# Performance work log

Measured on AMD Instinct MI355X. Metric: run time of the kernel, lower is better.

## Reference

```python
import jax, jax.numpy as jnp
import numpy as np

# Paged/ragged causal prefill attention (FlashInfer wrapper.run semantics),
# modeled as equal-length batched causal GQA attention.
B, S = 2, 2048          # batch, seq_len (T = B*S tokens, flattened)
H, HKV, D = 32, 8, 128  # query heads, kv heads, head dim
G = H // HKV            # GQA group size
SCALE = 0.08838834764831845  # 1/sqrt(D)


def setup_inputs() -> dict:
    key = jax.random.key(0)
    kq, kk, kv = jax.random.split(key, 3)
    q = jax.random.normal(kq, (B * S, H * D), dtype=jnp.float32)
    k = jax.random.normal(kk, (B * S, HKV * D), dtype=jnp.float32)
    v = jax.random.normal(kv, (B * S, HKV * D), dtype=jnp.float32)
    return {"q": q, "k": k, "v": v}


def reference(q, k, v):
    # q: [T, H*D] -> [B, S, HKV, G, D]; k, v: [T, HKV*D] -> [B, S, HKV, D]
    qh = q.reshape(B, S, HKV, G, D)
    kh = k.reshape(B, S, HKV, D)
    vh = v.reshape(B, S, HKV, D)
    # GQA attention scores: [B, HKV, G, Sq, Sk]
    scores = jnp.einsum('bqhgd,bkhd->bhgqk', qh, kh) * SCALE
    causal = jnp.tril(jnp.ones((S, S), dtype=bool))  # query attends to keys <= its position
    scores = jnp.where(causal, scores, jnp.finfo(scores.dtype).min)
    probs = jax.nn.softmax(scores, axis=-1)
    out = jnp.einsum('bhgqk,bkhd->bqhgd', probs, vh)
    # back to flattened token layout [T, H*D]
    return out.reshape(B * S, H * D)
```

## Files before the change

### kernel.cpp

```cpp
#include <hip/hip_runtime.h>


#define B_   2
#define S_   2048
#define H_   32
#define HKV_ 8
#define D_   128
#define SCALEF 0.08838834764831845f
#define COEF  (SCALEF * 1.44269504088896340736f)
#define DEFER_THR 8.0f

typedef float          f32x4 __attribute__((ext_vector_type(4)));
typedef __bf16         bf16x2 __attribute__((ext_vector_type(2)));
typedef __bf16         bf16x8 __attribute__((ext_vector_type(8)));
typedef unsigned short u16x8 __attribute__((ext_vector_type(8)));

#define MFMA16(a, b, c) __builtin_amdgcn_mfma_f32_16x16x32_bf16((a), (b), (c), 0, 0, 0)

#if defined(__has_builtin)
#if __has_builtin(__builtin_amdgcn_exp2f)
#define EXP2F(x) __builtin_amdgcn_exp2f(x)
#endif
#endif
#ifndef EXP2F
#define EXP2F(x) exp2f(x)
#endif

static __device__ __forceinline__ unsigned short f2bf(float f) {
  unsigned int u = __builtin_bit_cast(unsigned int, f);
  u = (u + 0x7fffu + ((u >> 16) & 1u)) >> 16;
  return (unsigned short)u;
}

static __device__ __forceinline__ void load_lds16(const void* g, void* l) {
  __builtin_amdgcn_global_load_lds(
      (const __attribute__((address_space(1))) void*)g,
      (__attribute__((address_space(3))) void*)l, 16, 0, 0);
}

template <int CTRL>
static __device__ __forceinline__ float dppf(float v) {
  return __builtin_bit_cast(
      float, __builtin_amdgcn_update_dpp(0, __builtin_bit_cast(int, v), CTRL,
                                         0xF, 0xF, true));
}
static __device__ __forceinline__ float rowmax16(float v) {
  v = fmaxf(v, dppf<0x128>(v));
  v = fmaxf(v, dppf<0x124>(v));
  v = fmaxf(v, dppf<0x122>(v));
  v = fmaxf(v, dppf<0x121>(v));
  return v;
}
static __device__ __forceinline__ float rowsum16(float v) {
  v += dppf<0x128>(v);
  v += dppf<0x124>(v);
  v += dppf<0x122>(v);
  v += dppf<0x121>(v);
  return v;
}

__global__ __launch_bounds__(256) void k_convert_kernel(
    const float* __restrict__ k, unsigned short* __restrict__ kbf) {
  int t = blockIdx.x * 256 + threadIdx.x;
  int o = t * 8;
  int d = o & (D_ - 1);
  int s = (o >> 7) & (S_ - 1);
  int bh = o >> 18;
  int b = bh >> 3, hkv = bh & 7;
  const float* src = k + (size_t)(b * S_ + s) * (HKV_ * D_) + hkv * D_ + d;
  f32x4 x0 = *(const f32x4*)src;
  f32x4 x1 = *(const f32x4*)(src + 4);
  u16x8 w;
  w[0] = f2bf(x0[0]); w[1] = f2bf(x0[1]); w[2] = f2bf(x0[2]); w[3] = f2bf(x0[3]);
  w[4] = f2bf(x1[0]); w[5] = f2bf(x1[1]); w[6] = f2bf(x1[2]); w[7] = f2bf(x1[3]);
  *(u16x8*)(kbf + o) = w;
}

__global__ __launch_bounds__(256) void vt_transpose_kernel(
    const float* __restrict__ v, unsigned short* __restrict__ vt) {
  __shared__ float tile[32][65];
  const int tid = threadIdx.x;
  const int s0 = blockIdx.x * 64;
  const int d0 = blockIdx.y * 32;
  const int bh = blockIdx.z;
  const float* src = v + (size_t)(bh >> 3) * S_ * (HKV_ * D_) + (bh & 7) * D_;
#pragma unroll
  for (int it = 0; it < 8; ++it) {
    int idx = it * 256 + tid;
    int sl = idx >> 5, dl = idx & 31;
    tile[dl][sl] = src[(size_t)(s0 + sl) * (HKV_ * D_) + d0 + dl];
  }
  __syncthreads();
  unsigned int* dst = (unsigned int*)vt;
#pragma unroll
  for (int it = 0; it < 4; ++it) {
    int idx = it * 256 + tid;
    int dl = idx >> 5, sp = idx & 31;
    unsigned int w = (unsigned int)f2bf(tile[dl][2 * sp]) |
                     ((unsigned int)f2bf(tile[dl][2 * sp + 1]) << 16);
    dst[(((size_t)bh * D_ + d0 + dl) * S_ + s0 + 2 * sp) >> 1] = w;
  }
}

#define PSTR 40

__global__ __launch_bounds__(256, 4) void attn_kernel(
    const float* __restrict__ qg, const unsigned short* __restrict__ kbfg,
    const unsigned short* __restrict__ vtg, float* __restrict__ outg) {
  __shared__ unsigned short KL[2][32 * 128];
  __shared__ unsigned short VL[2][128 * 32];
  __shared__ unsigned short PL[4][16 * PSTR];

  const int tid = threadIdx.x;
  const int wave = tid >> 6, lane = tid & 63;
  const int l15 = lane & 15, quad = lane >> 4;

  const int xb = (int)blockIdx.x;
  const int b = (int)(blockIdx.y >> 5), h = (int)(blockIdx.y & 31);
  const int hkv = h >> 2;

  const unsigned short* kbf = kbfg + (size_t)(b * HKV_ + hkv) * S_ * D_;
  const unsigned short* vtb = vtg + (size_t)(b * HKV_ + hkv) * D_ * S_;

  const f32x4 zero4 = {0.f, 0.f, 0.f, 0.f};
  const float NEG_INF = -__builtin_huge_valf();

  auto stage = [&](int kt, int buf) {
#pragma unroll
    for (int j = 0; j < 2; ++j) {
      int si = wave * 128 + j * 64 + lane;
      int kr = si >> 4, pc = si & 15;
      int lc = pc ^ (kr & 15);
      load_lds16(kbf + (size_t)(kt * 32 + kr) * D_ + lc * 8,
                 &KL[buf][(wave * 128 + j * 64) * 8]);
    }
#pragma unroll
    for (int j = 0; j < 2; ++j) {
      int si = wave * 128 + j * 64 + lane;
      int dr = si >> 2, pc = si & 3;
      int lc = pc ^ ((dr >> 1) & 3);
      load_lds16(vtb + (size_t)dr * S_ + kt * 32 + lc * 8,
                 &VL[buf][(wave * 128 + j * 64) * 8]);
    }
  };

  for (int ph = 0; ph < 2; ++ph) {
    const int qb = ph ? (31 - xb) : xb;
    const int qbase = qb * 64 + wave * 16;

    bf16x8 qf[4];
#pragma unroll
    for (int ch = 0; ch < 4; ++ch) {
      const float* p = qg + (size_t)(b * S_ + qbase + l15) * (H_ * D_) +
                       h * D_ + ch * 32 + quad * 8;
      f32x4 x0 = *(const f32x4*)p;
      f32x4 x1 = *(const f32x4*)(p + 4);
      bf16x8 t;
      t[0] = (__bf16)(x0[0] * COEF); t[1] = (__bf16)(x0[1] * COEF);
      t[2] = (__bf16)(x0[2] * COEF); t[3] = (__bf16)(x0[3] * COEF);
      t[4] = (__bf16)(x1[0] * COEF); t[5] = (__bf16)(x1[1] * COEF);
      t[6] = (__bf16)(x1[2] * COEF); t[7] = (__bf16)(x1[3] * COEF);
      qf[ch] = t;
    }

    f32x4 acc[8];
#pragma unroll
    for (int dt = 0; dt < 8; ++dt) acc[dt] = zero4;
    f32x4 mrow = {NEG_INF, NEG_INF, NEG_INF, NEG_INF};
    f32x4 lsum = zero4;
    float mmin = NEG_INF;

    const int nkt = qb * 2 + 2;

    stage(0, 0);
    __syncthreads();

#define KITER(KT, CUR)                                                        \
  do {                                                                        \
    const int kt_ = (KT);                                                     \
    if (kt_ + 1 < nkt) stage(kt_ + 1, (CUR) ^ 1);                             \
    if (kt_ * 32 <= qbase + 15) {                                             \
      f32x4 sc[2] = {zero4, zero4};                                           \
      __builtin_amdgcn_s_setprio(1);                                          \
      _Pragma("unroll") for (int h2 = 0; h2 < 2; ++h2) {                      \
        const int row = h2 * 16 + l15;                                        \
        _Pragma("unroll") for (int ch = 0; ch < 4; ++ch) {                    \
          const int pc = (ch * 4 + quad) ^ l15;               \
          u16x8 kf = *(const u16x8*)&KL[(CUR)][row * D_ + pc * 8];            \
          sc[h2] = MFMA16(qf[ch], __builtin_bit_cast(bf16x8, kf), sc[h2]);    \
        }                                                                     \
      }                                                                       \
      __builtin_amdgcn_s_setprio(0);                                          \
      const int kb0 = kt_ * 32;                                               \
      _Pragma("unroll") for (int h2 = 0; h2 < 2; ++h2) {                      \
        if (kb0 + h2 * 16 + 15 > qbase) {                                     \
          int kgp = kb0 + h2 * 16 + l15;                                      \
          _Pragma("unroll") for (int r = 0; r < 4; ++r) {                     \
            int qgp = qbase + quad * 4 + r;                                   \
            if (kgp > qgp) sc[h2][r] = NEG_INF;                               \
          }                                                                   \
        }                                                                     \
      }                                                                       \
        \
      {                                                                       \
        float t01 = fmaxf(fmaxf(sc[0][0], sc[1][0]),                          \
                          fmaxf(sc[0][1], sc[1][1]));                         \
        float t23 = fmaxf(fmaxf(sc[0][2], sc[1][2]),                          \
                          fmaxf(sc[0][3], sc[1][3]));                         \
        float dmax = fmaxf(t01, t23);                                         \
        if (!__all(dmax <= mmin + DEFER_THR)) {                               \
          f32x4 al;                                                           \
          _Pragma("unroll") for (int r = 0; r < 4; ++r) {                     \
            float mt = rowmax16(fmaxf(sc[0][r], sc[1][r]));                   \
            float mn = fmaxf(mrow[r], mt);                                    \
            al[r] = EXP2F(mrow[r] - mn);                                      \
            mrow[r] = mn;                                                     \
            lsum[r] *= al[r];                                                 \
          }                                                                   \
          _Pragma("unroll") for (int dt = 0; dt < 8; ++dt)                    \
              _Pragma("unroll") for (int r = 0; r < 4; ++r)                   \
                  acc[dt][r] *= al[r];                                        \
          mmin = fminf(fminf(mrow[0], mrow[1]), fminf(mrow[2], mrow[3]));     \
        }                                                                     \
      }                                                                       \
                         \
      _Pragma("unroll") for (int r = 0; r < 4; ++r) {                         \
        float p0 = EXP2F(sc[0][r] - mrow[r]);                                 \
        float p1 = EXP2F(sc[1][r] - mrow[r]);                                 \
        sc[0][r] = p0;                                                        \
        sc[1][r] = p1;                                                        \
        lsum[r] += p0 + p1;                                                   \
      }                                                                       \
           \
      _Pragma("unroll") for (int h2 = 0; h2 < 2; ++h2)                        \
          _Pragma("unroll") for (int r = 0; r < 4; ++r) {                     \
        float mine = sc[h2][r];                                               \
        float nb = dppf<0xB1>(mine);                                          \
        if (!(l15 & 1)) {                                                     \
          bf16x2 pk;                                                          \
          pk[0] = (__bf16)mine;                                               \
          pk[1] = (__bf16)nb;                                                 \
          *(bf16x2*)&PL[wave][(quad * 4 + r) * PSTR + h2 * 16 + l15] = pk;    \
        }                                                                     \
      }                                                                       \
                 \
      {                                                                       \
        u16x8 pf = *(const u16x8*)&PL[wave][l15 * PSTR + quad * 8];           \
        bf16x8 pb = __builtin_bit_cast(bf16x8, pf);                           \
        const int vsw = (quad ^ ((l15 >> 1) & 3)) * 8;                        \
        __builtin_amdgcn_s_setprio(1);                                        \
        _Pragma("unroll") for (int dt = 0; dt < 8; ++dt) {                    \
          u16x8 vf = *(const u16x8*)&VL[(CUR)][(dt * 16 + l15) * 32 + vsw];   \
          acc[dt] = MFMA16(pb, __builtin_bit_cast(bf16x8, vf), acc[dt]);      \
        }                                                                     \
        __builtin_amdgcn_s_setprio(0);                                        \
      }                                                                       \
    }                                                                         \
    __syncthreads();  \
  } while (0)

    for (int kt = 0; kt < nkt; kt += 2) {
      KITER(kt, 0);
      KITER(kt + 1, 1);
    }
#undef KITER

    f32x4 inv;
#pragma unroll
    for (int r = 0; r < 4; ++r) inv[r] = 1.0f / rowsum16(lsum[r]);
#pragma unroll
    for (int dt = 0; dt < 8; ++dt)
#pragma unroll
      for (int r = 0; r < 4; ++r)
        outg[(size_t)(b * S_ + qbase + quad * 4 + r) * (H_ * D_) +
             h * D_ + dt * 16 + l15] = acc[dt][r] * inv[r];
  }
}

extern "C" void kernel_launch(void* const* d_in, const int* in_sizes, int n_in,
                              void* d_out, int out_size, void* d_ws,
                              size_t ws_size, hipStream_t stream) {
  const float* q = (const float*)d_in[0];
  const float* k = (const float*)d_in[1];
  const float* v = (const float*)d_in[2];
  float* out = (float*)d_out;
  unsigned short* kws = (unsigned short*)d_ws;
  unsigned short* vtws = kws + (size_t)B_ * HKV_ * S_ * D_;

  k_convert_kernel<<<(B_ * S_ * HKV_ * D_ / 8) / 256, 256, 0, stream>>>(k, kws);

  dim3 g1(S_ / 64, D_ / 32, B_ * HKV_);
  vt_transpose_kernel<<<g1, 256, 0, stream>>>(v, vtws);

  dim3 g2(16, B_ * H_);
  attn_kernel<<<g2, 256, 0, stream>>>(q, kws, vtws, out);
}
```

Before: 240.9 us.

## Transpose QK^T MFMA so each lane owns one query row for softmax

The QK^T MFMA operands are swapped so the score tile is transposed: each lane now holds scores for a single query row across keys. Row max and row sum then need only a ds_swizzle plus one bpermute across quads, replacing four DPP steps per row. P is written to LDS as two bf16x4 stores with no DPP neighbour exchange or lane predication, using a narrower padded stride. The rescale factor has to be redistributed to the accumulator layout with bpermutes, and P is read back as two 8-byte loads, which adds LDS traffic and may bring bank conflicts.

```diff
diff --git a/kernel.cpp b/kernel.cpp
--- a/kernel.cpp
+++ b/kernel.cpp
@@ -11,7 +11,7 @@
 #define DEFER_THR 8.0f
 
 typedef float          f32x4 __attribute__((ext_vector_type(4)));
-typedef __bf16         bf16x2 __attribute__((ext_vector_type(2)));
+typedef __bf16         bf16x4 __attribute__((ext_vector_type(4)));
 typedef __bf16         bf16x8 __attribute__((ext_vector_type(8)));
 typedef unsigned short u16x8 __attribute__((ext_vector_type(8)));
 
@@ -38,25 +38,14 @@
       (__attribute__((address_space(3))) void*)l, 16, 0, 0);
 }
 
-template <int CTRL>
-static __device__ __forceinline__ float dppf(float v) {
+static __device__ __forceinline__ float swz_x16(float v) {
   return __builtin_bit_cast(
-      float, __builtin_amdgcn_update_dpp(0, __builtin_bit_cast(int, v), CTRL,
-                                         0xF, 0xF, true));
-}
-static __device__ __forceinline__ float rowmax16(float v) {
-  v = fmaxf(v, dppf<0x128>(v));
-  v = fmaxf(v, dppf<0x124>(v));
-  v = fmaxf(v, dppf<0x122>(v));
-  v = fmaxf(v, dppf<0x121>(v));
-  return v;
-}
-static __device__ __forceinline__ float rowsum16(float v) {
-  v += dppf<0x128>(v);
-  v += dppf<0x124>(v);
-  v += dppf<0x122>(v);
-  v += dppf<0x121>(v);
-  return v;
+      float, __builtin_amdgcn_ds_swizzle(__builtin_bit_cast(int, v), 0x401F));
+}
+static __device__ __forceinline__ float bperm_f(int byteaddr, float v) {
+  return __builtin_bit_cast(
+      float,
+      __builtin_amdgcn_ds_bpermute(byteaddr, __builtin_bit_cast(int, v)));
 }
 
 __global__ __launch_bounds__(256) void k_convert_kernel(
@@ -102,7 +91,7 @@
   }
 }
 
-#define PSTR 40
+#define PSTR 36
 
 __global__ __launch_bounds__(256, 4) void attn_kernel(
     const float* __restrict__ qg, const unsigned short* __restrict__ kbfg,
@@ -114,6 +103,8 @@
   const int tid = threadIdx.x;
   const int wave = tid >> 6, lane = tid & 63;
   const int l15 = lane & 15, quad = lane >> 4;
+  const int a32 = ((lane ^ 32) << 2);
+  const int rowa = quad << 4;
 
   const int xb = (int)blockIdx.x;
   const int b = (int)(blockIdx.y >> 5), h = (int)(blockIdx.y & 31);
@@ -147,6 +138,7 @@
   for (int ph = 0; ph < 2; ++ph) {
     const int qb = ph ? (31 - xb) : xb;
     const int qbase = qb * 64 + wave * 16;
+    const int qgp = qbase + l15;
 
     bf16x8 qf[4];
 #pragma unroll
@@ -166,9 +158,8 @@
     f32x4 acc[8];
 #pragma unroll
     for (int dt = 0; dt < 8; ++dt) acc[dt] = zero4;
-    f32x4 mrow = {NEG_INF, NEG_INF, NEG_INF, NEG_INF};
-    f32x4 lsum = zero4;
-    float mmin = NEG_INF;
+    float mrow = NEG_INF;
+    float lsum = 0.f;
 
     const int nkt = qb * 2 + 2;
 
@@ -187,66 +178,60 @@
         _Pragma("unroll") for (int ch = 0; ch < 4; ++ch) {                    \
           const int pc = (ch * 4 + quad) ^ l15;               \
           u16x8 kf = *(const u16x8*)&KL[(CUR)][row * D_ + pc * 8];            \
-          sc[h2] = MFMA16(qf[ch], __builtin_bit_cast(bf16x8, kf), sc[h2]);    \
+          sc[h2] = MFMA16(__builtin_bit_cast(bf16x8, kf), qf[ch], sc[h2]);    \
         }                                                                     \
       }                                                                       \
       __builtin_amdgcn_s_setprio(0);                                          \
       const int kb0 = kt_ * 32;                                               \
+          \
       _Pragma("unroll") for (int h2 = 0; h2 < 2; ++h2) {                      \
         if (kb0 + h2 * 16 + 15 > qbase) {                                     \
-          int kgp = kb0 + h2 * 16 + l15;                                      \
+          int kb2 = kb0 + h2 * 16 + quad * 4;                                 \
           _Pragma("unroll") for (int r = 0; r < 4; ++r) {                     \
-            int qgp = qbase + quad * 4 + r;                                   \
-            if (kgp > qgp) sc[h2][r] = NEG_INF;                               \
+            if (kb2 + r > qgp) sc[h2][r] = NEG_INF;                           \
           }                                                                   \
         }                                                                     \
       }                                                                       \
-        \
+         \
+      float l8 = fmaxf(fmaxf(fmaxf(sc[0][0], sc[0][1]),                       \
+                             fmaxf(sc[0][2], sc[0][3])),                      \
+                       fmaxf(fmaxf(sc[1][0], sc[1][1]),                       \
+                             fmaxf(sc[1][2], sc[1][3])));                     \
+      if (!__all(l8 <= mrow + DEFER_THR)) {                                   \
+        float t = fmaxf(l8, swz_x16(l8));             \
+        t = fmaxf(t, bperm_f(a32, t));                                        \
+        float mn = fmaxf(mrow, t);                                            \
+        float al = EXP2F(mrow - mn);                                          \
+        mrow = mn;                                                            \
+        lsum *= al;                                                           \
+        f32x4 av;       \
+        _Pragma("unroll") for (int r = 0; r < 4; ++r)                         \
+            av[r] = bperm_f(rowa + (r << 2), al);                             \
+        _Pragma("unroll") for (int dt = 0; dt < 8; ++dt)                      \
+            _Pragma("unroll") for (int r = 0; r < 4; ++r)                     \
+                acc[dt][r] *= av[r];                                          \
+      }                                                                       \
+                         \
+      _Pragma("unroll") for (int h2 = 0; h2 < 2; ++h2)                        \
+          _Pragma("unroll") for (int r = 0; r < 4; ++r)                       \
+              sc[h2][r] = EXP2F(sc[h2][r] - mrow);                            \
+      lsum += ((sc[0][0] + sc[0][1]) + (sc[0][2] + sc[0][3])) +               \
+              ((sc[1][0] + sc[1][1]) + (sc[1][2] + sc[1][3]));                \
+            \
       {                                                                       \
-        float t01 = fmaxf(fmaxf(sc[0][0], sc[1][0]),                          \
-                          fmaxf(sc[0][1], sc[1][1]));                         \
-        float t23 = fmaxf(fmaxf(sc[0][2], sc[1][2]),                          \
-                          fmaxf(sc[0][3], sc[1][3]));                         \
-        float dmax = fmaxf(t01, t23);                                         \
-        if (!__all(dmax <= mmin + DEFER_THR)) {                               \
-          f32x4 al;                                                           \
-          _Pragma("unroll") for (int r = 0; r < 4; ++r) {                     \
-            float mt = rowmax16(fmaxf(sc[0][r], sc[1][r]));                   \
-            float mn = fmaxf(mrow[r], mt);                                    \
-            al[r] = EXP2F(mrow[r] - mn);                                      \
-            mrow[r] = mn;                                                     \
-            lsum[r] *= al[r];                                                 \
-          }                                                                   \
-          _Pragma("unroll") for (int dt = 0; dt < 8; ++dt)                    \
-              _Pragma("unroll") for (int r = 0; r < 4; ++r)                   \
-                  acc[dt][r] *= al[r];                                        \
-          mmin = fminf(fminf(mrow[0], mrow[1]), fminf(mrow[2], mrow[3]));     \
-        }                                                                     \
-      }                                                                       \
-                         \
-      _Pragma("unroll") for (int r = 0; r < 4; ++r) {                         \
-        float p0 = EXP2F(sc[0][r] - mrow[r]);                                 \
-        float p1 = EXP2F(sc[1][r] - mrow[r]);                                 \
-        sc[0][r] = p0;                                                        \
-        sc[1][r] = p1;                                                        \
-        lsum[r] += p0 + p1;                                                   \
-      }                                                                       \
-           \
-      _Pragma("unroll") for (int h2 = 0; h2 < 2; ++h2)                        \
-          _Pragma("unroll") for (int r = 0; r < 4; ++r) {                     \
-        float mine = sc[h2][r];                                               \
-        float nb = dppf<0xB1>(mine);                                          \
-        if (!(l15 & 1)) {                                                     \
-          bf16x2 pk;                                                          \
-          pk[0] = (__bf16)mine;                                               \
-          pk[1] = (__bf16)nb;                                                 \
-          *(bf16x2*)&PL[wave][(quad * 4 + r) * PSTR + h2 * 16 + l15] = pk;    \
-        }                                                                     \
-      }                                                                       \
-                 \
+        bf16x4 w0, w1;                                                        \
+        w0[0] = (__bf16)sc[0][0]; w0[1] = (__bf16)sc[0][1];                   \
+        w0[2] = (__bf16)sc[0][2]; w0[3] = (__bf16)sc[0][3];                   \
+        w1[0] = (__bf16)sc[1][0]; w1[1] = (__bf16)sc[1][1];                   \
+        w1[2] = (__bf16)sc[1][2]; w1[3] = (__bf16)sc[1][3];                   \
+        *(bf16x4*)&PL[wave][l15 * PSTR + quad * 4] = w0;                      \
+        *(bf16x4*)&PL[wave][l15 * PSTR + 16 + quad * 4] = w1;                 \
+      }                                                                       \
+             \
       {                                                                       \
-        u16x8 pf = *(const u16x8*)&PL[wave][l15 * PSTR + quad * 8];           \
-        bf16x8 pb = __builtin_bit_cast(bf16x8, pf);                           \
+        bf16x4 p0 = *(const bf16x4*)&PL[wave][l15 * PSTR + quad * 8];         \
+        bf16x4 p1 = *(const bf16x4*)&PL[wave][l15 * PSTR + quad * 8 + 4];     \
+        bf16x8 pb = __builtin_shufflevector(p0, p1, 0, 1, 2, 3, 4, 5, 6, 7);  \
         const int vsw = (quad ^ ((l15 >> 1) & 3)) * 8;                        \
         __builtin_amdgcn_s_setprio(1);                                        \
         _Pragma("unroll") for (int dt = 0; dt < 8; ++dt) {                    \
@@ -265,9 +250,13 @@
     }
 #undef KITER
 
+    float s = lsum;
+    s += swz_x16(s);
+    s += bperm_f(a32, s);
+    float linv = 1.0f / s;
     f32x4 inv;
 #pragma unroll
-    for (int r = 0; r < 4; ++r) inv[r] = 1.0f / rowsum16(lsum[r]);
+    for (int r = 0; r < 4; ++r) inv[r] = bperm_f(rowa + (r << 2), linv);
 #pragma unroll
     for (int dt = 0; dt < 8; ++dt)
 #pragma unroll
```

Result: faster. 233.2 us (-3.2%).
